# Kernel optimization log

Measured on AMD Instinct MI355X. Metric: run time of the kernel, lower is better.

Reference implementation:

```python
import math
import jax, jax.numpy as jnp
import numpy as np

B, H, S, D = 2, 16, 2048, 64

def setup_inputs() -> dict:
    key = jax.random.key(0)
    kq, kk, kv, km = jax.random.split(key, 4)
    q = jax.random.normal(kq, (B, H, S, D), dtype=jnp.float32)
    k = jax.random.normal(kk, (B, H, S, D), dtype=jnp.float32)
    v = jax.random.normal(kv, (B, H, S, D), dtype=jnp.float32)
    mask = jax.random.randint(km, (B, S, S), 0, 2, dtype=jnp.int32)
    return {"q": q, "k": k, "v": v, "mask": mask}

def reference(q, k, v, mask):
    # attn = q @ (k^T / sqrt(d))  -> [B,H,Sq,Sk]
    scale = 1.0 / math.sqrt(q.shape[-1])
    attn = jnp.einsum("bhqd,bhkd->bhqk", q, k * scale)
    # masked_fill where mask.unsqueeze(1) == 1
    attn = jnp.where(mask[:, None, :, :] == 1, jnp.float32(-1e9), attn)
    attn = jax.nn.softmax(attn, axis=-1)
    # dropout is identity in eval / p=0
    res = jnp.einsum("bhqk,bhkd->bhqd", attn, v)
    return (res, attn)
```

## Files before the change

### kernel.cpp

```cpp
#include <hip/hip_runtime.h>

#define B_ 2
#define H_ 16
#define S_ 2048
#define D_ 64
#define QB 32
#define KT 64
#define NTHREADS 512

typedef _Float16 f16;
typedef _Float16 f16x8 __attribute__((ext_vector_type(8)));
typedef _Float16 f16x4 __attribute__((ext_vector_type(4)));
typedef _Float16 f16x2 __attribute__((ext_vector_type(2)));
typedef float f32x4 __attribute__((ext_vector_type(4)));

#define MFMA16(a, b, c) __builtin_amdgcn_mfma_f32_16x16x32_f16(a, b, c, 0, 0, 0)

__global__ __launch_bounds__(NTHREADS)
void attn_kernel(const float* __restrict__ q, const float* __restrict__ k,
                 const float* __restrict__ v, const int* __restrict__ mask,
                 float* __restrict__ out)
{
    __shared__ f16 Qsh[QB][D_ + 8];
    __shared__ f16 Ksh[KT][D_ + 8];
    __shared__ f16 Vsh[KT][D_ + 2];
    __shared__ f16 Psh[QB][KT + 8];
    __shared__ float rowred[QB];
    __shared__ float rlsh[QB];

    const int tid  = threadIdx.x;
    const int wave = tid >> 6;
    const int lane = tid & 63;
    const int quad = lane >> 4;
    const int l16  = lane & 15;
    const int qi   = wave & 1;
    const int ni   = wave >> 1;

    const int qb = blockIdx.x;
    const int h  = blockIdx.y;
    const int b  = blockIdx.z;
    const int bh = b * H_ + h;

    const float* Qg = q + ((size_t)bh * S_ + (size_t)qb * QB) * D_;
    const float* Kg = k + (size_t)bh * S_ * D_;
    const float* Vg = v + (size_t)bh * S_ * D_;
    const int*   Mg = mask + ((size_t)b * S_ + (size_t)qb * QB) * S_;
    float* res_out  = out + ((size_t)bh * S_ + (size_t)qb * QB) * D_;
    float* attn_out = out + (size_t)B_ * H_ * S_ * D_
                          + ((size_t)bh * S_ + (size_t)qb * QB) * S_;

    if (tid < QB) rowred[tid] = 0.f;

    {
        const int row = tid >> 4;
        const int c4  = (tid & 15) * 4;
        const float4 qv = *(const float4*)(Qg + row * D_ + c4);
        f16x4 o;
        o[0] = (f16)(qv.x * 0.125f); o[1] = (f16)(qv.y * 0.125f);
        o[2] = (f16)(qv.z * 0.125f); o[3] = (f16)(qv.w * 0.125f);
        *(f16x4*)&Qsh[row][c4] = o;
    }
    __syncthreads();

    const int qrow0 = qi * 16 + quad * 4;
    const f16x8 a0 = *(const f16x8*)&Qsh[qi * 16 + l16][quad * 8];
    const f16x8 a1 = *(const f16x8*)&Qsh[qi * 16 + l16][32 + quad * 8];

    const int colbase = ni * 16 + l16;
    const int* mp0 = Mg + (size_t)qrow0 * S_ + colbase;

    const int skk = tid >> 3;
    const int sd0 = (tid & 7) * 8;

    float psum[4] = {0.f, 0.f, 0.f, 0.f};
    for (int kt = 0; kt < S_ / KT; ++kt) {
        {
            const float* src = Kg + ((size_t)(kt * KT + skk)) * D_ + sd0;
            const float4 x0 = *(const float4*)(src);
            const float4 x1 = *(const float4*)(src + 4);
            f16x8 o;
            o[0] = (f16)x0.x; o[1] = (f16)x0.y; o[2] = (f16)x0.z; o[3] = (f16)x0.w;
            o[4] = (f16)x1.x; o[5] = (f16)x1.y; o[6] = (f16)x1.z; o[7] = (f16)x1.w;
            *(f16x8*)&Ksh[skk][sd0] = o;
        }
        __syncthreads();
        const f16x8 b0 = *(const f16x8*)&Ksh[ni * 16 + l16][quad * 8];
        const f16x8 b1 = *(const f16x8*)&Ksh[ni * 16 + l16][32 + quad * 8];
        f32x4 c = {0.f, 0.f, 0.f, 0.f};
        c = MFMA16(a0, b0, c);
        c = MFMA16(a1, b1, c);
        const int* mp = mp0 + kt * KT;
#pragma unroll
        for (int r = 0; r < 4; ++r) {
            const int m = mp[(size_t)r * S_];
            const float e = (m == 1) ? 0.f : __expf(c[r]);
            psum[r] += e;
        }
        __syncthreads();
    }

#pragma unroll
    for (int r = 0; r < 4; ++r) {
        psum[r] += __shfl_xor(psum[r], 1);
        psum[r] += __shfl_xor(psum[r], 2);
        psum[r] += __shfl_xor(psum[r], 4);
        psum[r] += __shfl_xor(psum[r], 8);
    }
    if (l16 == 0) {
#pragma unroll
        for (int r = 0; r < 4; ++r) atomicAdd(&rowred[qrow0 + r], psum[r]);
    }
    __syncthreads();
    if (tid < QB) rlsh[tid] = 1.0f / rowred[tid];
    __syncthreads();
    float rlq[4];
#pragma unroll
    for (int r = 0; r < 4; ++r) rlq[r] = rlsh[qrow0 + r];

    f32x4 oacc = {0.f, 0.f, 0.f, 0.f};
    float* ap0 = attn_out + (size_t)qrow0 * S_ + colbase;

    for (int kt = 0; kt < S_ / KT; ++kt) {
        {
            const float* srck = Kg + ((size_t)(kt * KT + skk)) * D_ + sd0;
            const float4 x0 = *(const float4*)(srck);
            const float4 x1 = *(const float4*)(srck + 4);
            f16x8 o;
            o[0] = (f16)x0.x; o[1] = (f16)x0.y; o[2] = (f16)x0.z; o[3] = (f16)x0.w;
            o[4] = (f16)x1.x; o[5] = (f16)x1.y; o[6] = (f16)x1.z; o[7] = (f16)x1.w;
            *(f16x8*)&Ksh[skk][sd0] = o;

            const float* srcv = Vg + ((size_t)(kt * KT + skk)) * D_ + sd0;
            const float4 y0 = *(const float4*)(srcv);
            const float4 y1 = *(const float4*)(srcv + 4);
            f16x2 p01, p23, p45, p67;
            p01[0] = (f16)y0.x; p01[1] = (f16)y0.y;
            p23[0] = (f16)y0.z; p23[1] = (f16)y0.w;
            p45[0] = (f16)y1.x; p45[1] = (f16)y1.y;
            p67[0] = (f16)y1.z; p67[1] = (f16)y1.w;
            *(f16x2*)&Vsh[skk][sd0]     = p01;
            *(f16x2*)&Vsh[skk][sd0 + 2] = p23;
            *(f16x2*)&Vsh[skk][sd0 + 4] = p45;
            *(f16x2*)&Vsh[skk][sd0 + 6] = p67;
        }
        __syncthreads();
        const f16x8 b0 = *(const f16x8*)&Ksh[ni * 16 + l16][quad * 8];
        const f16x8 b1 = *(const f16x8*)&Ksh[ni * 16 + l16][32 + quad * 8];
        f32x4 c = {0.f, 0.f, 0.f, 0.f};
        c = MFMA16(a0, b0, c);
        c = MFMA16(a1, b1, c);
        const int* mp = mp0 + kt * KT;
        float* ap = ap0 + kt * KT;
#pragma unroll
        for (int r = 0; r < 4; ++r) {
            const int m = mp[(size_t)r * S_];
            const float e = (m == 1) ? 0.f : __expf(c[r]);
            const float p = e * rlq[r];
            ap[(size_t)r * S_] = p;
            Psh[qrow0 + r][colbase] = (f16)p;
        }
        __syncthreads();
        const f16x8 pa0 = *(const f16x8*)&Psh[qi * 16 + l16][quad * 8];
        const f16x8 pa1 = *(const f16x8*)&Psh[qi * 16 + l16][32 + quad * 8];
        f16x8 vb0, vb1;
        const int dcol = ni * 16 + l16;
#pragma unroll
        for (int j = 0; j < 8; ++j) {
            vb0[j] = Vsh[quad * 8 + j][dcol];
            vb1[j] = Vsh[32 + quad * 8 + j][dcol];
        }
        oacc = MFMA16(pa0, vb0, oacc);
        oacc = MFMA16(pa1, vb1, oacc);
        __syncthreads();
    }

#pragma unroll
    for (int r = 0; r < 4; ++r)
        res_out[(size_t)(qrow0 + r) * D_ + ni * 16 + l16] = oacc[r];
}

extern "C" void kernel_launch(void* const* d_in, const int* in_sizes, int n_in,
                              void* d_out, int out_size, void* d_ws, size_t ws_size,
                              hipStream_t stream) {
    (void)in_sizes; (void)n_in; (void)out_size; (void)d_ws; (void)ws_size;
    const float* q   = (const float*)d_in[0];
    const float* k   = (const float*)d_in[1];
    const float* v   = (const float*)d_in[2];
    const int*  mask = (const int*)d_in[3];
    float* out = (float*)d_out;
    dim3 grid(S_ / QB, H_, B_);
    attn_kernel<<<grid, dim3(NTHREADS), 0, stream>>>(q, k, v, mask, out);
}
```

Baseline: 839.7 us.

## Double-buffer K/V tiles, prefetch mask, and store V transposed in LDS

```diff
diff --git a/kernel.cpp b/kernel.cpp
--- a/kernel.cpp
+++ b/kernel.cpp
@@ -6,6 +6,7 @@
 #define D_ 64
 #define QB 32
 #define KT 64
+#define NT (S_ / KT)
 #define NTHREADS 512
 
 typedef _Float16 f16;
@@ -22,9 +23,9 @@
                  float* __restrict__ out)
 {
     __shared__ f16 Qsh[QB][D_ + 8];
-    __shared__ f16 Ksh[KT][D_ + 8];
-    __shared__ f16 Vsh[KT][D_ + 2];
-    __shared__ f16 Psh[QB][KT + 8];
+    __shared__ f16 Ksh[2][KT][D_ + 8];
+    __shared__ f16 Vt [2][D_][KT + 8];
+    __shared__ f16 Psh[2][QB][KT + 8];
     __shared__ float rowred[QB];
     __shared__ float rlsh[QB];
 
@@ -60,41 +61,61 @@
         o[2] = (f16)(qv.z * 0.125f); o[3] = (f16)(qv.w * 0.125f);
         *(f16x4*)&Qsh[row][c4] = o;
     }
-    __syncthreads();
-
-    const int qrow0 = qi * 16 + quad * 4;
+
+    const int skk = tid >> 3;
+    const int sd0 = (tid & 7) * 8;
+    const int vkp = tid & 31;
+    const int vd0 = (tid >> 5) * 4;
+
+    const int qrow0   = qi * 16 + quad * 4;
+    const int colbase = ni * 16 + l16;
+    const int* mp0 = Mg + (size_t)qrow0 * S_ + colbase;
+
+    {
+        const float* src = Kg + (size_t)skk * D_ + sd0;
+        const float4 x0 = *(const float4*)(src);
+        const float4 x1 = *(const float4*)(src + 4);
+        f16x8 o;
+        o[0] = (f16)x0.x; o[1] = (f16)x0.y; o[2] = (f16)x0.z; o[3] = (f16)x0.w;
+        o[4] = (f16)x1.x; o[5] = (f16)x1.y; o[6] = (f16)x1.z; o[7] = (f16)x1.w;
+        *(f16x8*)&Ksh[0][skk][sd0] = o;
+    }
+    int mnext[4];
+#pragma unroll
+    for (int r = 0; r < 4; ++r) mnext[r] = mp0[(size_t)r * S_];
+    __syncthreads();
+
     const f16x8 a0 = *(const f16x8*)&Qsh[qi * 16 + l16][quad * 8];
     const f16x8 a1 = *(const f16x8*)&Qsh[qi * 16 + l16][32 + quad * 8];
 
-    const int colbase = ni * 16 + l16;
-    const int* mp0 = Mg + (size_t)qrow0 * S_ + colbase;
-
-    const int skk = tid >> 3;
-    const int sd0 = (tid & 7) * 8;
-
     float psum[4] = {0.f, 0.f, 0.f, 0.f};
-    for (int kt = 0; kt < S_ / KT; ++kt) {
+    for (int kt = 0; kt < NT; ++kt) {
+        const int cur = kt & 1;
+        const int ktn = (kt + 1 < NT) ? kt + 1 : kt;
+        const float* srck = Kg + ((size_t)(ktn * KT + skk)) * D_ + sd0;
+        const float4 x0 = *(const float4*)(srck);
+        const float4 x1 = *(const float4*)(srck + 4);
+        int mcur[4];
+#pragma unroll
+        for (int r = 0; r < 4; ++r) mcur[r] = mnext[r];
+        const int* mpn = mp0 + ktn * KT;
+#pragma unroll
+        for (int r = 0; r < 4; ++r) mnext[r] = mpn[(size_t)r * S_];
+
+        const f16x8 b0 = *(const f16x8*)&Ksh[cur][ni * 16 + l16][quad * 8];
+        const f16x8 b1 = *(const f16x8*)&Ksh[cur][ni * 16 + l16][32 + quad * 8];
+        f32x4 c = {0.f, 0.f, 0.f, 0.f};
+        c = MFMA16(a0, b0, c);
+        c = MFMA16(a1, b1, c);
+#pragma unroll
+        for (int r = 0; r < 4; ++r)
+            psum[r] += (mcur[r] == 1) ? 0.f : __expf(c[r]);
+
         {
-            const float* src = Kg + ((size_t)(kt * KT + skk)) * D_ + sd0;
-            const float4 x0 = *(const float4*)(src);
-            const float4 x1 = *(const float4*)(src + 4);
             f16x8 o;
             o[0] = (f16)x0.x; o[1] = (f16)x0.y; o[2] = (f16)x0.z; o[3] = (f16)x0.w;
             o[4] = (f16)x1.x; o[5] = (f16)x1.y; o[6] = (f16)x1.z; o[7] = (f16)x1.w;
-            *(f16x8*)&Ksh[skk][sd0] = o;
-        }
-        __syncthreads();
-        const f16x8 b0 = *(const f16x8*)&Ksh[ni * 16 + l16][quad * 8];
-        const f16x8 b1 = *(const f16x8*)&Ksh[ni * 16 + l16][32 + quad * 8];
-        f32x4 c = {0.f, 0.f, 0.f, 0.f};
-        c = MFMA16(a0, b0, c);
-        c = MFMA16(a1, b1, c);
-        const int* mp = mp0 + kt * KT;
-#pragma unroll
-        for (int r = 0; r < 4; ++r) {
-            const int m = mp[(size_t)r * S_];
-            const float e = (m == 1) ? 0.f : __expf(c[r]);
-            psum[r] += e;
+            *(f16x8*)&Ksh[cur ^ 1][skk][sd0] = o;
         }
         __syncthreads();
     }
@@ -117,60 +138,87 @@
 #pragma unroll
     for (int r = 0; r < 4; ++r) rlq[r] = rlsh[qrow0 + r];
 
+    {
+        const float* srck = Kg + (size_t)skk * D_ + sd0;
+        const float4 x0 = *(const float4*)(srck);
+        const float4 x1 = *(const float4*)(srck + 4);
+        f16x8 o;
+        o[0] = (f16)x0.x; o[1] = (f16)x0.y; o[2] = (f16)x0.z; o[3] = (f16)x0.w;
+        o[4] = (f16)x1.x; o[5] = (f16)x1.y; o[6] = (f16)x1.z; o[7] = (f16)x1.w;
+        *(f16x8*)&Ksh[0][skk][sd0] = o;
+
+        const float* srcv = Vg + (size_t)(2 * vkp) * D_ + vd0;
+        const float4 y0 = *(const float4*)(srcv);
+        const float4 y1 = *(const float4*)(srcv + D_);
+#pragma unroll
+        for (int j = 0; j < 4; ++j) {
+            f16x2 pr;
+            pr[0] = (f16)((&y0.x)[j]);
+            pr[1] = (f16)((&y1.x)[j]);
+            *(f16x2*)&Vt[0][vd0 + j][2 * vkp] = pr;
+        }
+#pragma unroll
+        for (int r = 0; r < 4; ++r) mnext[r] = mp0[(size_t)r * S_];
+    }
+    __syncthreads();
+
     f32x4 oacc = {0.f, 0.f, 0.f, 0.f};
     float* ap0 = attn_out + (size_t)qrow0 * S_ + colbase;
-
-    for (int kt = 0; kt < S_ / KT; ++kt) {
+    const int dcol = colbase;
+
+    for (int kt = 0; kt < NT; ++kt) {
+        const int cur = kt & 1;
+        const int nxt = cur ^ 1;
+        const int ktn = (kt + 1 < NT) ? kt + 1 : kt;
+
+        const float* srck = Kg + ((size_t)(ktn * KT + skk)) * D_ + sd0;
+        const float4 x0 = *(const float4*)(srck);
+        const float4 x1 = *(const float4*)(srck + 4);
+        const float* srcv = Vg + ((size_t)(ktn * KT + 2 * vkp)) * D_ + vd0;
+        const float4 y0 = *(const float4*)(srcv);
+        const float4 y1 = *(const float4*)(srcv + D_);
+        int mcur[4];
+#pragma unroll
+        for (int r = 0; r < 4; ++r) mcur[r] = mnext[r];
+        const int* mpn = mp0 + ktn * KT;
+#pragma unroll
+        for (int r = 0; r < 4; ++r) mnext[r] = mpn[(size_t)r * S_];
+
+        const f16x8 b0 = *(const f16x8*)&Ksh[cur][ni * 16 + l16][quad * 8];
+        const f16x8 b1 = *(const f16x8*)&Ksh[cur][ni * 16 + l16][32 + quad * 8];
+        f32x4 c = {0.f, 0.f, 0.f, 0.f};
+        c = MFMA16(a0, b0, c);
+        c = MFMA16(a1, b1, c);
+        float* ap = ap0 + kt * KT;
+#pragma unroll
+        for (int r = 0; r < 4; ++r) {
+            const float e = (mcur[r] == 1) ? 0.f : __expf(c[r]);
+            const float p = e * rlq[r];
+            ap[(size_t)r * S_] = p;
+            Psh[cur][qrow0 + r][colbase] = (f16)p;
+        }
+        __syncthreads();
+
+        const f16x8 pa0 = *(const f16x8*)&Psh[cur][qi * 16 + l16][quad * 8];
+        const f16x8 pa1 = *(const f16x8*)&Psh[cur][qi * 16 + l16][32 + quad * 8];
+        const f16x8 vb0 = *(const f16x8*)&Vt[cur][dcol][quad * 8];
+        const f16x8 vb1 = *(const f16x8*)&Vt[cur][dcol][32 + quad * 8];
+        oacc = MFMA16(pa0, vb0, oacc);
+        oacc = MFMA16(pa1, vb1, oacc);
+
         {
-            const float* srck = Kg + ((size_t)(kt * KT + skk)) * D_ + sd0;
-            const float4 x0 = *(const float4*)(srck);
-            const float4 x1 = *(const float4*)(srck + 4);
             f16x8 o;
             o[0] = (f16)x0.x; o[1] = (f16)x0.y; o[2] = (f16)x0.z; o[3] = (f16)x0.w;
             o[4] = (f16)x1.x; o[5] = (f16)x1.y; o[6] = (f16)x1.z; o[7] = (f16)x1.w;
-            *(f16x8*)&Ksh[skk][sd0] = o;
-
-            const float* srcv = Vg + ((size_t)(kt * KT + skk)) * D_ + sd0;
-            const float4 y0 = *(const float4*)(srcv);
-            const float4 y1 = *(const float4*)(srcv + 4);
-            f16x2 p01, p23, p45, p67;
-            p01[0] = (f16)y0.x; p01[1] = (f16)y0.y;
-            p23[0] = (f16)y0.z; p23[1] = (f16)y0.w;
-            p45[0] = (f16)y1.x; p45[1] = (f16)y1.y;
-            p67[0] = (f16)y1.z; p67[1] = (f16)y1.w;
-            *(f16x2*)&Vsh[skk][sd0]     = p01;
-            *(f16x2*)&Vsh[skk][sd0 + 2] = p23;
-            *(f16x2*)&Vsh[skk][sd0 + 4] = p45;
-            *(f16x2*)&Vsh[skk][sd0 + 6] = p67;
-        }
-        __syncthreads();
-        const f16x8 b0 = *(const f16x8*)&Ksh[ni * 16 + l16][quad * 8];
-        const f16x8 b1 = *(const f16x8*)&Ksh[ni * 16 + l16][32 + quad * 8];
-        f32x4 c = {0.f, 0.f, 0.f, 0.f};
-        c = MFMA16(a0, b0, c);
-        c = MFMA16(a1, b1, c);
-        const int* mp = mp0 + kt * KT;
-        float* ap = ap0 + kt * KT;
-#pragma unroll
-        for (int r = 0; r < 4; ++r) {
-            const int m = mp[(size_t)r * S_];
-            const float e = (m == 1) ? 0.f : __expf(c[r]);
-            const float p = e * rlq[r];
-            ap[(size_t)r * S_] = p;
-            Psh[qrow0 + r][colbase] = (f16)p;
-        }
-        __syncthreads();
-        const f16x8 pa0 = *(const f16x8*)&Psh[qi * 16 + l16][quad * 8];
-        const f16x8 pa1 = *(const f16x8*)&Psh[qi * 16 + l16][32 + quad * 8];
-        f16x8 vb0, vb1;
-        const int dcol = ni * 16 + l16;
-#pragma unroll
-        for (int j = 0; j < 8; ++j) {
-            vb0[j] = Vsh[quad * 8 + j][dcol];
-            vb1[j] = Vsh[32 + quad * 8 + j][dcol];
-        }
-        oacc = MFMA16(pa0, vb0, oacc);
-        oacc = MFMA16(pa1, vb1, oacc);
+            *(f16x8*)&Ksh[nxt][skk][sd0] = o;
+        }
+#pragma unroll
+        for (int j = 0; j < 4; ++j) {
+            f16x2 pr;
+            pr[0] = (f16)((&y0.x)[j]);
+            pr[1] = (f16)((&y1.x)[j]);
+            *(f16x2*)&Vt[nxt][vd0 + j][2 * vkp] = pr;
+        }
         __syncthreads();
     }
 
```

Result: slower. 933.8 us (+11.2%).

## Double query block to 64 rows so each wave computes a 16x32 tile

Applied to the files above, without the earlier changes.

```diff
diff --git a/kernel.cpp b/kernel.cpp
--- a/kernel.cpp
+++ b/kernel.cpp
@@ -4,7 +4,7 @@
 #define H_ 16
 #define S_ 2048
 #define D_ 64
-#define QB 32
+#define QB 64
 #define KT 64
 #define NTHREADS 512
 
@@ -33,8 +33,8 @@
     const int lane = tid & 63;
     const int quad = lane >> 4;
     const int l16  = lane & 15;
-    const int qi   = wave & 1;
-    const int ni   = wave >> 1;
+    const int qi   = wave & 3;
+    const int ni   = wave >> 2;
 
     const int qb = blockIdx.x;
     const int h  = blockIdx.y;
@@ -52,13 +52,16 @@
     if (tid < QB) rowred[tid] = 0.f;
 
     {
-        const int row = tid >> 4;
-        const int c4  = (tid & 15) * 4;
-        const float4 qv = *(const float4*)(Qg + row * D_ + c4);
-        f16x4 o;
-        o[0] = (f16)(qv.x * 0.125f); o[1] = (f16)(qv.y * 0.125f);
-        o[2] = (f16)(qv.z * 0.125f); o[3] = (f16)(qv.w * 0.125f);
-        *(f16x4*)&Qsh[row][c4] = o;
+        const int row = tid >> 3;
+        const int c   = (tid & 7) * 8;
+        const float4 q0 = *(const float4*)(Qg + row * D_ + c);
+        const float4 q1 = *(const float4*)(Qg + row * D_ + c + 4);
+        f16x8 o;
+        o[0] = (f16)(q0.x * 0.125f); o[1] = (f16)(q0.y * 0.125f);
+        o[2] = (f16)(q0.z * 0.125f); o[3] = (f16)(q0.w * 0.125f);
+        o[4] = (f16)(q1.x * 0.125f); o[5] = (f16)(q1.y * 0.125f);
+        o[6] = (f16)(q1.z * 0.125f); o[7] = (f16)(q1.w * 0.125f);
+        *(f16x8*)&Qsh[row][c] = o;
     }
     __syncthreads();
 
@@ -84,17 +87,23 @@
             *(f16x8*)&Ksh[skk][sd0] = o;
         }
         __syncthreads();
-        const f16x8 b0 = *(const f16x8*)&Ksh[ni * 16 + l16][quad * 8];
-        const f16x8 b1 = *(const f16x8*)&Ksh[ni * 16 + l16][32 + quad * 8];
-        f32x4 c = {0.f, 0.f, 0.f, 0.f};
-        c = MFMA16(a0, b0, c);
-        c = MFMA16(a1, b1, c);
+        const f16x8 b0a = *(const f16x8*)&Ksh[colbase][quad * 8];
+        const f16x8 b0b = *(const f16x8*)&Ksh[colbase][32 + quad * 8];
+        const f16x8 b1a = *(const f16x8*)&Ksh[32 + colbase][quad * 8];
+        const f16x8 b1b = *(const f16x8*)&Ksh[32 + colbase][32 + quad * 8];
+        f32x4 c0 = {0.f, 0.f, 0.f, 0.f};
+        c0 = MFMA16(a0, b0a, c0);
+        c0 = MFMA16(a1, b0b, c0);
+        f32x4 c1 = {0.f, 0.f, 0.f, 0.f};
+        c1 = MFMA16(a0, b1a, c1);
+        c1 = MFMA16(a1, b1b, c1);
         const int* mp = mp0 + kt * KT;
 #pragma unroll
         for (int r = 0; r < 4; ++r) {
-            const int m = mp[(size_t)r * S_];
-            const float e = (m == 1) ? 0.f : __expf(c[r]);
-            psum[r] += e;
+            const int m0 = mp[(size_t)r * S_];
+            const int m1 = mp[(size_t)r * S_ + 32];
+            psum[r] += (m0 == 1) ? 0.f : __expf(c0[r]);
+            psum[r] += (m1 == 1) ? 0.f : __expf(c1[r]);
         }
         __syncthreads();
     }
@@ -117,7 +126,8 @@
 #pragma unroll
     for (int r = 0; r < 4; ++r) rlq[r] = rlsh[qrow0 + r];
 
-    f32x4 oacc = {0.f, 0.f, 0.f, 0.f};
+    f32x4 oaccA = {0.f, 0.f, 0.f, 0.f};
+    f32x4 oaccB = {0.f, 0.f, 0.f, 0.f};
     float* ap0 = attn_out + (size_t)qrow0 * S_ + colbase;
 
     for (int kt = 0; kt < S_ / KT; ++kt) {
@@ -144,39 +154,56 @@
             *(f16x2*)&Vsh[skk][sd0 + 6] = p67;
         }
         __syncthreads();
-        const f16x8 b0 = *(const f16x8*)&Ksh[ni * 16 + l16][quad * 8];
-        const f16x8 b1 = *(const f16x8*)&Ksh[ni * 16 + l16][32 + quad * 8];
-        f32x4 c = {0.f, 0.f, 0.f, 0.f};
-        c = MFMA16(a0, b0, c);
-        c = MFMA16(a1, b1, c);
+        const f16x8 b0a = *(const f16x8*)&Ksh[colbase][quad * 8];
+        const f16x8 b0b = *(const f16x8*)&Ksh[colbase][32 + quad * 8];
+        const f16x8 b1a = *(const f16x8*)&Ksh[32 + colbase][quad * 8];
+        const f16x8 b1b = *(const f16x8*)&Ksh[32 + colbase][32 + quad * 8];
+        f32x4 c0 = {0.f, 0.f, 0.f, 0.f};
+        c0 = MFMA16(a0, b0a, c0);
+        c0 = MFMA16(a1, b0b, c0);
+        f32x4 c1 = {0.f, 0.f, 0.f, 0.f};
+        c1 = MFMA16(a0, b1a, c1);
+        c1 = MFMA16(a1, b1b, c1);
         const int* mp = mp0 + kt * KT;
         float* ap = ap0 + kt * KT;
 #pragma unroll
         for (int r = 0; r < 4; ++r) {
-            const int m = mp[(size_t)r * S_];
-            const float e = (m == 1) ? 0.f : __expf(c[r]);
-            const float p = e * rlq[r];
-            ap[(size_t)r * S_] = p;
-            Psh[qrow0 + r][colbase] = (f16)p;
+            const int m0 = mp[(size_t)r * S_];
+            const int m1 = mp[(size_t)r * S_ + 32];
+            const float e0 = (m0 == 1) ? 0.f : __expf(c0[r]);
+            const float e1 = (m1 == 1) ? 0.f : __expf(c1[r]);
+            const float p0 = e0 * rlq[r];
+            const float p1 = e1 * rlq[r];
+            ap[(size_t)r * S_]      = p0;
+            ap[(size_t)r * S_ + 32] = p1;
+            Psh[qrow0 + r][colbase]      = (f16)p0;
+            Psh[qrow0 + r][colbase + 32] = (f16)p1;
         }
         __syncthreads();
         const f16x8 pa0 = *(const f16x8*)&Psh[qi * 16 + l16][quad * 8];
         const f16x8 pa1 = *(const f16x8*)&Psh[qi * 16 + l16][32 + quad * 8];
-        f16x8 vb0, vb1;
-        const int dcol = ni * 16 + l16;
+        f16x8 vb0a, vb1a, vb0b, vb1b;
+        const int dcolA = colbase;
+        const int dcolB = colbase + 32;
 #pragma unroll
         for (int j = 0; j < 8; ++j) {
-            vb0[j] = Vsh[quad * 8 + j][dcol];
-            vb1[j] = Vsh[32 + quad * 8 + j][dcol];
-        }
-        oacc = MFMA16(pa0, vb0, oacc);
-        oacc = MFMA16(pa1, vb1, oacc);
-        __syncthreads();
-    }
-
-#pragma unroll
-    for (int r = 0; r < 4; ++r)
-        res_out[(size_t)(qrow0 + r) * D_ + ni * 16 + l16] = oacc[r];
+            vb0a[j] = Vsh[quad * 8 + j][dcolA];
+            vb1a[j] = Vsh[32 + quad * 8 + j][dcolA];
+            vb0b[j] = Vsh[quad * 8 + j][dcolB];
+            vb1b[j] = Vsh[32 + quad * 8 + j][dcolB];
+        }
+        oaccA = MFMA16(pa0, vb0a, oaccA);
+        oaccA = MFMA16(pa1, vb1a, oaccA);
+        oaccB = MFMA16(pa0, vb0b, oaccB);
+        oaccB = MFMA16(pa1, vb1b, oaccB);
+        __syncthreads();
+    }
+
+#pragma unroll
+    for (int r = 0; r < 4; ++r) {
+        res_out[(size_t)(qrow0 + r) * D_ + colbase]      = oaccA[r];
+        res_out[(size_t)(qrow0 + r) * D_ + colbase + 32] = oaccB[r];
+    }
 }
 
 extern "C" void kernel_launch(void* const* d_in, const int* in_sizes, int n_in,
```

After: 836.7 us. No clear change (-0.4%).
